# Kernel optimization log

Measured on AMD Instinct MI355X. Metric: run time of the kernel, lower is better.

Reference implementation:

```python
import jax, jax.numpy as jnp
import numpy as np

N_NODES = 50000
N_EDGES = 1600000
N_GRAPHS = 128
EDGE_DIM = 43
IN_DIM = 35
H = 128          # hidden_dim_1 = hidden_dim_2 = hidden_dim_3
G1, G2 = 64, 32  # gate MLP dims
H6, H7, H8 = 256, 128, 64
U0, U1 = 64, 64  # u_shape


def _linear_params(key, out_dim, in_dim):
    k1, k2 = jax.random.split(key)
    bound = 1.0 / np.sqrt(in_dim)
    W = jax.random.uniform(k1, (out_dim, in_dim), minval=-bound, maxval=bound, dtype=jnp.float32)
    b = jax.random.uniform(k2, (out_dim,), minval=-bound, maxval=bound, dtype=jnp.float32)
    return W, b


def setup_inputs() -> dict:
    key = jax.random.key(0)
    ks = jax.random.split(key, 24)
    x = jax.random.normal(ks[0], (N_NODES, IN_DIM), dtype=jnp.float32)
    edge_index = jax.random.randint(ks[1], (2, N_EDGES), 0, N_NODES, dtype=jnp.int64)
    edge_attr = jax.random.normal(ks[2], (N_EDGES, EDGE_DIM), dtype=jnp.float32)
    batch = jnp.sort(jax.random.randint(ks[3], (N_NODES,), 0, N_GRAPHS, dtype=jnp.int64))
    batch = batch.at[0].set(0).at[-1].set(N_GRAPHS - 1)
    u_soap = jax.random.normal(ks[4], (N_GRAPHS, U0), dtype=jnp.float32)
    u_dimer = jax.random.normal(ks[5], (N_GRAPHS, U1), dtype=jnp.float32)

    W1n, b1n = _linear_params(ks[6], H, IN_DIM + EDGE_DIM)
    W1r, b1r = _linear_params(ks[7], H, IN_DIM)
    W2n, b2n = _linear_params(ks[8], H, H + EDGE_DIM)
    W2r, b2r = _linear_params(ks[9], H, H)
    W3n, b3n = _linear_params(ks[10], H, H + EDGE_DIM)
    W3r, b3r = _linear_params(ks[11], H, H)
    Wg1, bg1 = _linear_params(ks[12], G1, H)
    Wg2, bg2 = _linear_params(ks[13], G2, G1)
    Wg3, bg3 = _linear_params(ks[14], 1, G2)
    Wl1, bl1 = _linear_params(ks[15], H6, U0 + U1 + H)
    Wl2, bl2 = _linear_params(ks[16], H7, H6)
    Wl3, bl3 = _linear_params(ks[17], H8, H7)
    Wl, bl = _linear_params(ks[18], 4, H8)

    return dict(x=x, edge_attr=edge_attr, u_soap=u_soap, u_dimer=u_dimer,
                W1n=W1n, b1n=b1n, W1r=W1r, b1r=b1r,
                W2n=W2n, b2n=b2n, W2r=W2r, b2r=b2r,
                W3n=W3n, b3n=b3n, W3r=W3r, b3r=b3r,
                Wg1=Wg1, bg1=bg1, Wg2=Wg2, bg2=bg2, Wg3=Wg3, bg3=bg3,
                Wl1=Wl1, bl1=bl1, Wl2=Wl2, bl2=bl2, Wl3=Wl3, bl3=bl3,
                Wl=Wl, bl=bl,
                edge_index=edge_index, batch=batch)


def _conv(x, src, edge_attr, Wn, bn, Wr, br):
    # gather source nodes, concat edge features, linear + tanh, scatter-add back to SOURCE (as in original)
    x_adj = jnp.tanh(jnp.concatenate([x[src], edge_attr], axis=1) @ Wn.T + bn)  # [E, H]
    neg_sum = jax.ops.segment_sum(x_adj, src, num_segments=N_NODES)             # [N, H]
    return jnp.tanh(x @ Wr.T + br) + neg_sum


def _segment_softmax(gate, batch, num_segments):
    m = jax.ops.segment_max(gate[:, 0], batch, num_segments=num_segments)
    g = jnp.exp(gate[:, 0] - m[batch])
    s = jax.ops.segment_sum(g, batch, num_segments=num_segments)
    return (g / (s[batch] + 1e-16))[:, None]


def reference(x, edge_attr, u_soap, u_dimer,
              W1n, b1n, W1r, b1r, W2n, b2n, W2r, b2r, W3n, b3n, W3r, b3r,
              Wg1, bg1, Wg2, bg2, Wg3, bg3,
              Wl1, bl1, Wl2, bl2, Wl3, bl3, Wl, bl,
              edge_index, batch):
    src = edge_index[0]
    h = _conv(x, src, edge_attr, W1n, b1n, W1r, b1r)
    h = _conv(h, src, edge_attr, W2n, b2n, W2r, b2r)
    h = _conv(h, src, edge_attr, W3n, b3n, W3r, b3r)

    # GlobalAttention readout
    g = jax.nn.relu(h @ Wg1.T + bg1)
    g = jax.nn.relu(g @ Wg2.T + bg2)
    gate = g @ Wg3.T + bg3                             # [N, 1]
    att = _segment_softmax(gate, batch, N_GRAPHS)      # [N, 1]
    embedding = jax.ops.segment_sum(att * h, batch, num_segments=N_GRAPHS)  # [G, H]

    u = jnp.concatenate([u_soap[:, :U0], u_dimer[:, :U1]], axis=1)
    e2 = jnp.concatenate([embedding, u], axis=1)
    out = jax.nn.relu(e2 @ Wl1.T + bl1)
    out = jax.nn.relu(out @ Wl2.T + bl2)
    out = jax.nn.relu(out @ Wl3.T + bl3)
    out4 = out @ Wl.T + bl                             # [G, 4]
    pred_last = out4.sum(axis=1, keepdims=True)
    return jnp.concatenate([out4, pred_last], axis=1), att
```

## Files before the change

kernel.cpp:

```cpp
#include <hip/hip_runtime.h>
#include <cstdint>
#include <cstddef>

#define N_NODES_C 50000
#define N_EDGES_C 1600000
#define N_GRAPHS_C 128
#define EDGE_DIM_C 43
#define IN_DIM_C 35
#define HDIM_C 128
#define MAXG_C 150000

typedef _Float16 f16x8 __attribute__((ext_vector_type(8)));
typedef float f32x4 __attribute__((ext_vector_type(4)));

__device__ __forceinline__ float fast_tanh(float x) {
    float xc = fminf(9.0f, fmaxf(-9.0f, x));
    float t = __expf(2.0f * xc);
    return (t - 1.0f) * __builtin_amdgcn_rcpf(t + 1.0f);
}


__global__ __launch_bounds__(256) void hist_kernel(const int* __restrict__ src,
                                                   int* __restrict__ cnt) {
    int i = blockIdx.x * 256 + threadIdx.x;
    if (i < N_EDGES_C) atomicAdd(&cnt[src[i]], 1);
}

__global__ __launch_bounds__(1024) void scan_kernel(const int* __restrict__ cnt,
                                                    int* __restrict__ rowptr,
                                                    int* __restrict__ work,
                                                    int* __restrict__ growptr,
                                                    int* __restrict__ ngroups) {
    __shared__ int wsumA[16], wsumB[16];
    __shared__ int carryA, carryB;
    int t = threadIdx.x;
    int lane = t & 63, wid = t >> 6;
    if (t == 0) { carryA = 0; carryB = 0; }
    __syncthreads();
    for (int base = 0; base < N_NODES_C; base += 4096) {
        int i0 = base + t * 4;
        int v[4], u[4];
        #pragma unroll
        for (int j = 0; j < 4; ++j) {
            int i = i0 + j;
            v[j] = (i < N_NODES_C) ? cnt[i] : 0;
            u[j] = (v[j] + 15) >> 4;
        }
        int pv[4], pu[4];
        pv[0] = 0; pu[0] = 0;
        #pragma unroll
        for (int j = 1; j < 4; ++j) { pv[j] = pv[j-1] + v[j-1]; pu[j] = pu[j-1] + u[j-1]; }
        int tA = pv[3] + v[3], tB = pu[3] + u[3];
        int x = tA, y = tB;
        #pragma unroll
        for (int off = 1; off < 64; off <<= 1) {
            int xx = __shfl_up(x, off, 64);
            int yy = __shfl_up(y, off, 64);
            if (lane >= off) { x += xx; y += yy; }
        }
        if (lane == 63) { wsumA[wid] = x; wsumB[wid] = y; }
        __syncthreads();
        if (wid == 0) {
            int wa = (lane < 16) ? wsumA[lane] : 0;
            int wb = (lane < 16) ? wsumB[lane] : 0;
            #pragma unroll
            for (int off = 1; off < 16; off <<= 1) {
                int aa = __shfl_up(wa, off, 64);
                int bb = __shfl_up(wb, off, 64);
                if (lane >= off) { wa += aa; wb += bb; }
            }
            if (lane < 16) { wsumA[lane] = wa; wsumB[lane] = wb; }
        }
        __syncthreads();
        int exA = carryA + (wid ? wsumA[wid - 1] : 0) + x - tA;
        int exB = carryB + (wid ? wsumB[wid - 1] : 0) + y - tB;
        #pragma unroll
        for (int j = 0; j < 4; ++j) {
            int i = i0 + j;
            if (i < N_NODES_C) {
                int rv = exA + pv[j];
                rowptr[i] = rv; work[i] = rv;
                growptr[i] = exB + pu[j];
            }
        }
        int totA = wsumA[15], totB = wsumB[15];
        __syncthreads();
        if (t == 0) { carryA += totA; carryB += totB; }
        __syncthreads();
    }
    if (t == 0) {
        rowptr[N_NODES_C] = carryA;
        growptr[N_NODES_C] = carryB;
        ngroups[0] = carryB;
    }
}

__global__ __launch_bounds__(256) void scatter_kernel(const int* __restrict__ src,
                                                      int* __restrict__ work,
                                                      int* __restrict__ perm) {
    int i = blockIdx.x * 256 + threadIdx.x;
    if (i < N_EDGES_C) {
        int s = src[i];
        int pos = atomicAdd(&work[s], 1);
        perm[pos] = i;
    }
}

__global__ __launch_bounds__(256) void graph_misc(const int* __restrict__ rowptr,
                                                  const int* __restrict__ growptr,
                                                  const int* __restrict__ batch,
                                                  int2* __restrict__ nmeta,
                                                  int2* __restrict__ gmeta,
                                                  int* __restrict__ grp) {
    int i = blockIdx.x * 256 + threadIdx.x;
    if (i < N_NODES_C) {
        int r0 = rowptr[i], r1 = rowptr[i + 1];
        int g0 = growptr[i], g1 = growptr[i + 1];
        int deg = r1 - r0;
        nmeta[i] = make_int2(deg, g0);
        for (int g = g0; g < g1; ++g) {
            int o = (g - g0) * 16;
            int vv = deg - o; if (vv > 16) vv = 16;
            gmeta[g] = make_int2(r0 + o, vv);
        }
    }
    if (i <= N_GRAPHS_C) {
        int lo = 0, hi = N_NODES_C;
        while (lo < hi) {
            int mid = (lo + hi) >> 1;
            if (batch[mid] < i) lo = mid + 1; else hi = mid;
        }
        grp[i] = lo;
    }
}

__global__ __launch_bounds__(256) void permute_ea(const float* __restrict__ EA,
                                                  const int* __restrict__ perm,
                                                  const int2* __restrict__ gmeta,
                                                  const int* __restrict__ ngroups_p,
                                                  _Float16* __restrict__ EAp) {
    int t = threadIdx.x;
    int lane = t & 63, wid = t >> 6;
    int row = lane >> 2, q = lane & 3;
    int ng = ngroups_p[0];
    int gstride = gridDim.x * 4;
    for (int g = blockIdx.x * 4 + wid; g < ng; g += gstride) {
        int2 gm = gmeta[g];
        int ebase = gm.x, valid = gm.y;
        bool rv = row < valid;
        int e = rv ? perm[ebase + row] : 0;
        const float* pe = EA + (size_t)e * EDGE_DIM_C;
        unsigned int pk[6];
        #pragma unroll
        for (int jj = 0; jj < 6; ++jj) {
            int c0 = q * 12 + 2 * jj;
            float v0 = (rv && c0 < EDGE_DIM_C) ? pe[c0] : 0.0f;
            float v1 = (rv && c0 + 1 < EDGE_DIM_C) ? pe[c0 + 1] : 0.0f;
            unsigned short h0 = __builtin_bit_cast(unsigned short, (_Float16)v0);
            unsigned short h1 = __builtin_bit_cast(unsigned short, (_Float16)v1);
            pk[jj] = (unsigned int)h0 | ((unsigned int)h1 << 16);
        }
        unsigned int* outp = (unsigned int*)(EAp + (size_t)g * 768 + row * 48 + q * 12);
        *(uint2*)(outp)     = make_uint2(pk[0], pk[1]);
        *(uint2*)(outp + 2) = make_uint2(pk[2], pk[3]);
        *(uint2*)(outp + 4) = make_uint2(pk[4], pk[5]);
    }
}


#define BKN 32
__global__ __launch_bounds__(256) void node_gemm(
    const float* __restrict__ A, int K,
    const float* __restrict__ Wn, int ldn, const float* __restrict__ bn,
    const float* __restrict__ Wr, const float* __restrict__ br,
    float* __restrict__ Base, float* __restrict__ Root)
{
    __shared__ float At[BKN][64];
    __shared__ float Bw[BKN][128];
    int t = threadIdx.x;
    int z = blockIdx.y;
    const float* W = z ? Wr : Wn;
    int ldW = z ? K : ldn;
    const float* bias = z ? br : bn;
    float* Out = z ? Root : Base;

    int m0 = blockIdx.x * 64;
    int tn4 = (t % 32) * 4;
    int tm8 = (t / 32) * 8;
    float acc[8][4];
    #pragma unroll
    for (int a = 0; a < 8; a++)
        #pragma unroll
        for (int b = 0; b < 4; b++) acc[a][b] = 0.0f;

    int nkc = (K + BKN - 1) / BKN;
    for (int c = 0; c < nkc; c++) {
        int kc = c * BKN;
        {
            int m_l = t % 64;
            int kg = t / 64;
            int m = m0 + m_l;
            #pragma unroll
            for (int ii = 0; ii < 8; ii++) {
                int kk = kg * 8 + ii;
                int k = kc + kk;
                float v = 0.0f;
                if (m < N_NODES_C && k < K) v = A[(size_t)m * K + k];
                At[kk][m_l] = v;
            }
        }
        {
            int j = t % 128;
            int kg2 = t / 128;
            #pragma unroll
            for (int ii = 0; ii < 16; ii++) {
                int kk = kg2 * 16 + ii;
                int k = kc + kk;
                float v = 0.0f;
                if (k < K) v = W[(size_t)j * ldW + k];
                Bw[kk][j] = v;
            }
        }
        __syncthreads();
        #pragma unroll
        for (int kk = 0; kk < BKN; kk++) {
            float a[8], b[4];
            #pragma unroll
            for (int mi = 0; mi < 8; mi++) a[mi] = At[kk][tm8 + mi];
            #pragma unroll
            for (int ni = 0; ni < 4; ni++) b[ni] = Bw[kk][tn4 + ni];
            #pragma unroll
            for (int mi = 0; mi < 8; mi++)
                #pragma unroll
                for (int ni = 0; ni < 4; ni++)
                    acc[mi][ni] = fmaf(a[mi], b[ni], acc[mi][ni]);
        }
        __syncthreads();
    }

    float4 bv = *(const float4*)&bias[tn4];
    #pragma unroll
    for (int mi = 0; mi < 8; mi++) {
        int m = m0 + tm8 + mi;
        if (m < N_NODES_C) {
            float4 o;
            o.x = acc[mi][0] + bv.x;
            o.y = acc[mi][1] + bv.y;
            o.z = acc[mi][2] + bv.z;
            o.w = acc[mi][3] + bv.w;
            if (z) { o.x = fast_tanh(o.x); o.y = fast_tanh(o.y); o.z = fast_tanh(o.z); o.w = fast_tanh(o.w); }
            *(float4*)&Out[(size_t)m * HDIM_C + tn4] = o;
        }
    }
}


__global__ __launch_bounds__(256) void edge_mfma(
    const _Float16* __restrict__ EAp, const int2* __restrict__ nmeta,
    const float* __restrict__ Base, const float* __restrict__ Root,
    const float* __restrict__ Wfull, int colOff, int ldW,
    float* __restrict__ Hout)
{
    int t = threadIdx.x;
    int lane = t & 63, wid = t >> 6;
    int l15 = lane & 15, quad = lane >> 4;

    f16x8 bf[8][2];
    #pragma unroll
    for (int nt = 0; nt < 8; ++nt) {
        const float* wr = Wfull + (size_t)(nt * 16 + l15) * ldW + colOff;
        #pragma unroll
        for (int kt = 0; kt < 2; ++kt) {
            f16x8 b;
            #pragma unroll
            for (int j = 0; j < 8; ++j) {
                int k = kt * 32 + quad * 8 + j;
                float v = (k < EDGE_DIM_C) ? wr[k] : 0.0f;
                b[j] = (_Float16)v;
            }
            bf[nt][kt] = b;
        }
    }

    int nstride = gridDim.x * 4;
    for (int n = blockIdx.x * 4 + wid; n < N_NODES_C; n += nstride) {
        int2 nm = nmeta[n];
        int deg = nm.x, gptr = nm.y;
        const float* bp = Base + (size_t)n * HDIM_C;
        float bv[8];
        #pragma unroll
        for (int nt = 0; nt < 8; ++nt) bv[nt] = bp[nt * 16 + l15];
        float cs[8];
        #pragma unroll
        for (int nt = 0; nt < 8; ++nt) cs[nt] = 0.0f;

        int ngr = (deg + 15) >> 4;
        int rbase = quad * 4;
        for (int gi = 0; gi < ngr; ++gi) {
            int valid = deg - gi * 16; if (valid > 16) valid = 16;
            const _Float16* ap = EAp + (size_t)(gptr + gi) * 768 + l15 * 48;
            f16x8 a0 = *(const f16x8*)(ap + quad * 8);
            f16x8 a1;
            if (quad < 2) a1 = *(const f16x8*)(ap + 32 + quad * 8);
            else { f16x8 zz = {}; a1 = zz; }

            f32x4 acc[8];
            #pragma unroll
            for (int nt = 0; nt < 8; ++nt) {
                f32x4 zz = {0.f, 0.f, 0.f, 0.f};
                acc[nt] = __builtin_amdgcn_mfma_f32_16x16x32_f16(a0, bf[nt][0], zz, 0, 0, 0);
                acc[nt] = __builtin_amdgcn_mfma_f32_16x16x32_f16(a1, bf[nt][1], acc[nt], 0, 0, 0);
            }
            #pragma unroll
            for (int nt = 0; nt < 8; ++nt) {
                #pragma unroll
                for (int r = 0; r < 4; ++r) {
                    float v = fast_tanh(acc[nt][r] + bv[nt]);
                    cs[nt] += (rbase + r < valid) ? v : 0.0f;
                }
            }
        }
        #pragma unroll
        for (int nt = 0; nt < 8; ++nt) {
            cs[nt] += __shfl_xor(cs[nt], 16, 64);
            cs[nt] += __shfl_xor(cs[nt], 32, 64);
        }
        float v0, v1;
        if (quad == 0)      { v0 = cs[0]; v1 = cs[1]; }
        else if (quad == 1) { v0 = cs[2]; v1 = cs[3]; }
        else if (quad == 2) { v0 = cs[4]; v1 = cs[5]; }
        else                { v0 = cs[6]; v1 = cs[7]; }
        int c0 = quad * 32 + l15;
        size_t rowb = (size_t)n * HDIM_C;
        Hout[rowb + c0]      = Root[rowb + c0] + v0;
        Hout[rowb + c0 + 16] = Root[rowb + c0 + 16] + v1;
    }
}


__global__ __launch_bounds__(256) void gate_kernel(
    const float* __restrict__ h,
    const float* __restrict__ Wg1, const float* __restrict__ bg1,
    const float* __restrict__ Wg2, const float* __restrict__ bg2,
    const float* __restrict__ Wg3, const float* __restrict__ bg3,
    float* __restrict__ gate)
{
    __shared__ float Ht[128][65];
    __shared__ float G1[64][65];
    __shared__ float G2[32][65];
    int t = threadIdx.x;
    int m0 = blockIdx.x * 64;
    #pragma unroll
    for (int ii = 0; ii < 32; ++ii) {
        int flat = ii * 256 + t;
        int k = flat & 127, m = flat >> 7;
        float v = (m0 + m < N_NODES_C) ? h[(size_t)(m0 + m) * HDIM_C + k] : 0.0f;
        Ht[k][m] = v;
    }
    __syncthreads();
    int m = t & 63, slab = t >> 6;
    {
        float a[16];
        #pragma unroll
        for (int jj = 0; jj < 16; ++jj) a[jj] = bg1[slab * 16 + jj];
        for (int k = 0; k < 128; ++k) {
            float hv = Ht[k][m];
            #pragma unroll
            for (int jj = 0; jj < 16; ++jj)
                a[jj] = fmaf(Wg1[(size_t)(slab * 16 + jj) * 128 + k], hv, a[jj]);
        }
        #pragma unroll
        for (int jj = 0; jj < 16; ++jj) G1[slab * 16 + jj][m] = fmaxf(a[jj], 0.0f);
    }
    __syncthreads();
    {
        float b[8];
        #pragma unroll
        for (int jj = 0; jj < 8; ++jj) b[jj] = bg2[slab * 8 + jj];
        for (int k = 0; k < 64; ++k) {
            float gv = G1[k][m];
            #pragma unroll
            for (int jj = 0; jj < 8; ++jj)
                b[jj] = fmaf(Wg2[(size_t)(slab * 8 + jj) * 64 + k], gv, b[jj]);
        }
        #pragma unroll
        for (int jj = 0; jj < 8; ++jj) G2[slab * 8 + jj][m] = fmaxf(b[jj], 0.0f);
    }
    __syncthreads();
    if (t < 64 && m0 + t < N_NODES_C) {
        float s = bg3[0];
        #pragma unroll
        for (int k = 0; k < 32; ++k) s = fmaf(Wg3[k], G2[k][t], s);
        gate[m0 + t] = s;
    }
}


__global__ __launch_bounds__(256) void graph_attn(
    const float* __restrict__ gate, const int* __restrict__ grp,
    const float* __restrict__ h3, float* __restrict__ att_out,
    float* __restrict__ emb)
{
    int g = blockIdx.x;
    int t = threadIdx.x;
    int s = grp[g], e = grp[g + 1];
    __shared__ float red[256];
    __shared__ float attb[256];

    float m = -3.4e38f;
    for (int i = s + t; i < e; i += 256) m = fmaxf(m, gate[i]);
    red[t] = m;
    __syncthreads();
    #pragma unroll
    for (int off = 128; off >= 1; off >>= 1) {
        if (t < off) red[t] = fmaxf(red[t], red[t + off]);
        __syncthreads();
    }
    m = red[0];
    __syncthreads();

    float sum = 0.0f;
    for (int i = s + t; i < e; i += 256) sum += __expf(gate[i] - m);
    red[t] = sum;
    __syncthreads();
    #pragma unroll
    for (int off = 128; off >= 1; off >>= 1) {
        if (t < off) red[t] += red[t + off];
        __syncthreads();
    }
    float scale = 1.0f / (red[0] + 1e-16f);
    __syncthreads();

    int j = t & 127;
    int half = t >> 7;
    float acc = 0.0f;
    for (int base = s; base < e; base += 256) {
        int i = base + t;
        float a = 0.0f;
        if (i < e) {
            a = __expf(gate[i] - m) * scale;
            att_out[i] = a;
        }
        attb[t] = a;
        __syncthreads();
        int cnt = e - base; if (cnt > 256) cnt = 256;
        for (int r = half; r < cnt; r += 2)
            acc = fmaf(attb[r], h3[(size_t)(base + r) * HDIM_C + j], acc);
        __syncthreads();
    }
    red[t] = acc;
    __syncthreads();
    if (t < 128) emb[(size_t)g * 128 + t] = red[t] + red[t + 128];
}


__global__ __launch_bounds__(256) void final_mlp(
    const float* __restrict__ emb, const float* __restrict__ us, const float* __restrict__ ud,
    const float* __restrict__ Wl1, const float* __restrict__ bl1,
    const float* __restrict__ Wl2, const float* __restrict__ bl2,
    const float* __restrict__ Wl3, const float* __restrict__ bl3,
    const float* __restrict__ Wl, const float* __restrict__ bl,
    float* __restrict__ out5)
{
    int g = blockIdx.x;
    int t = threadIdx.x;
    __shared__ float e2[256], o1[256], o2[128], o3[64], o4[4];
    if (t < 128) e2[t] = emb[(size_t)g * 128 + t];
    else if (t < 192) e2[t] = us[(size_t)g * 64 + (t - 128)];
    else e2[t] = ud[(size_t)g * 64 + (t - 192)];
    __syncthreads();
    {
        float s = bl1[t];
        const float* wr = Wl1 + (size_t)t * 256;
        #pragma unroll 8
        for (int k = 0; k < 256; k++) s = fmaf(wr[k], e2[k], s);
        o1[t] = fmaxf(s, 0.0f);
    }
    __syncthreads();
    if (t < 128) {
        float s = bl2[t];
        const float* wr = Wl2 + (size_t)t * 256;
        #pragma unroll 8
        for (int k = 0; k < 256; k++) s = fmaf(wr[k], o1[k], s);
        o2[t] = fmaxf(s, 0.0f);
    }
    __syncthreads();
    if (t < 64) {
        float s = bl3[t];
        const float* wr = Wl3 + (size_t)t * 128;
        #pragma unroll 8
        for (int k = 0; k < 128; k++) s = fmaf(wr[k], o2[k], s);
        o3[t] = fmaxf(s, 0.0f);
    }
    __syncthreads();
    if (t < 4) {
        float s = bl[t];
        const float* wr = Wl + (size_t)t * 64;
        #pragma unroll 8
        for (int k = 0; k < 64; k++) s = fmaf(wr[k], o3[k], s);
        o4[t] = s;
    }
    __syncthreads();
    if (t < 5) {
        float v = (t < 4) ? o4[t] : (o4[0] + o4[1] + o4[2] + o4[3]);
        out5[(size_t)g * 5 + t] = v;
    }
}


extern "C" void kernel_launch(void* const* d_in, const int* in_sizes, int n_in,
                              void* d_out, int out_size, void* d_ws, size_t ws_size,
                              hipStream_t stream) {
    const float* x       = (const float*)d_in[0];
    const float* ea      = (const float*)d_in[1];
    const float* u_soap  = (const float*)d_in[2];
    const float* u_dimer = (const float*)d_in[3];
    const float* W1n = (const float*)d_in[4];   const float* b1n = (const float*)d_in[5];
    const float* W1r = (const float*)d_in[6];   const float* b1r = (const float*)d_in[7];
    const float* W2n = (const float*)d_in[8];   const float* b2n = (const float*)d_in[9];
    const float* W2r = (const float*)d_in[10];  const float* b2r = (const float*)d_in[11];
    const float* W3n = (const float*)d_in[12];  const float* b3n = (const float*)d_in[13];
    const float* W3r = (const float*)d_in[14];  const float* b3r = (const float*)d_in[15];
    const float* Wg1 = (const float*)d_in[16];  const float* bg1 = (const float*)d_in[17];
    const float* Wg2 = (const float*)d_in[18];  const float* bg2 = (const float*)d_in[19];
    const float* Wg3 = (const float*)d_in[20];  const float* bg3 = (const float*)d_in[21];
    const float* Wl1 = (const float*)d_in[22];  const float* bl1 = (const float*)d_in[23];
    const float* Wl2 = (const float*)d_in[24];  const float* bl2 = (const float*)d_in[25];
    const float* Wl3 = (const float*)d_in[26];  const float* bl3 = (const float*)d_in[27];
    const float* Wl  = (const float*)d_in[28];  const float* bl  = (const float*)d_in[29];
    const int* eidx  = (const int*)d_in[30];
    const int* batch = (const int*)d_in[31];
    const int* src = eidx;

    float* out5 = (float*)d_out;
    float* att  = out5 + (size_t)N_GRAPHS_C * 5;

    char* p = (char*)d_ws;
    size_t off = 0;
    auto alloc = [&](size_t bytes) -> void* {
        void* r = p + off;
        off += (bytes + 255) & ~(size_t)255;
        return r;
    };
    int* cnt     = (int*)alloc((size_t)N_NODES_C * 4);
    int* rowptr  = (int*)alloc((size_t)(N_NODES_C + 1) * 4);
    int* growptr = (int*)alloc((size_t)(N_NODES_C + 1) * 4);
    int* work    = (int*)alloc((size_t)N_NODES_C * 4);
    int* perm    = (int*)alloc((size_t)N_EDGES_C * 4);
    int* grp     = (int*)alloc((size_t)(N_GRAPHS_C + 1) * 4);
    int* ngroups = (int*)alloc(256);
    int2* nmeta  = (int2*)alloc((size_t)N_NODES_C * 8);
    int2* gmeta  = (int2*)alloc((size_t)MAXG_C * 8);
    float* gate  = (float*)alloc((size_t)N_NODES_C * 4);
    float* emb   = (float*)alloc((size_t)N_GRAPHS_C * 128 * 4);
    float* bufP  = (float*)alloc((size_t)N_NODES_C * HDIM_C * 4);
    float* bufQ  = (float*)alloc((size_t)N_NODES_C * HDIM_C * 4);
    float* bufR  = (float*)alloc((size_t)N_NODES_C * HDIM_C * 4);
    _Float16* EAp = (_Float16*)alloc((size_t)MAXG_C * 768 * 2);

    hipMemsetAsync(cnt, 0, (size_t)N_NODES_C * 4, stream);

    int eblocks = (N_EDGES_C + 255) / 256;
    hist_kernel<<<eblocks, 256, 0, stream>>>(src, cnt);
    scan_kernel<<<1, 1024, 0, stream>>>(cnt, rowptr, work, growptr, ngroups);
    scatter_kernel<<<eblocks, 256, 0, stream>>>(src, work, perm);
    graph_misc<<<(N_NODES_C + 255) / 256, 256, 0, stream>>>(rowptr, growptr, batch, nmeta, gmeta, grp);
    permute_ea<<<1536, 256, 0, stream>>>(ea, perm, gmeta, ngroups, EAp);

    dim3 ng((N_NODES_C + 63) / 64, 2);
    int egrid = 2048;

    node_gemm<<<ng, 256, 0, stream>>>(x, IN_DIM_C, W1n, IN_DIM_C + EDGE_DIM_C, b1n, W1r, b1r, bufP, bufQ);
    edge_mfma<<<egrid, 256, 0, stream>>>(EAp, nmeta, bufP, bufQ, W1n, IN_DIM_C, IN_DIM_C + EDGE_DIM_C, bufP);
    node_gemm<<<ng, 256, 0, stream>>>(bufP, HDIM_C, W2n, HDIM_C + EDGE_DIM_C, b2n, W2r, b2r, bufQ, bufR);
    edge_mfma<<<egrid, 256, 0, stream>>>(EAp, nmeta, bufQ, bufR, W2n, HDIM_C, HDIM_C + EDGE_DIM_C, bufQ);
    node_gemm<<<ng, 256, 0, stream>>>(bufQ, HDIM_C, W3n, HDIM_C + EDGE_DIM_C, b3n, W3r, b3r, bufP, bufR);
    edge_mfma<<<egrid, 256, 0, stream>>>(EAp, nmeta, bufP, bufR, W3n, HDIM_C, HDIM_C + EDGE_DIM_C, bufP);

    gate_kernel<<<(N_NODES_C + 63) / 64, 256, 0, stream>>>(bufP, Wg1, bg1, Wg2, bg2, Wg3, bg3, gate);
    graph_attn<<<N_GRAPHS_C, 256, 0, stream>>>(gate, grp, bufP, att, emb);
    final_mlp<<<N_GRAPHS_C, 256, 0, stream>>>(emb, u_soap, u_dimer,
                                              Wl1, bl1, Wl2, bl2, Wl3, bl3, Wl, bl, out5);
}
```

Baseline: 1.860 ms.

## Permute edge attributes by source-order scatter and prefetch next edge group

The edge-attribute packing now scatters: each edge reads its own row contiguously and writes it to its slot in the CSR layout. Before, each destination group gathered edges through a permutation array. This replaces the gmeta construction with an epos array plus a separate pad_zero kernel that clears the unused rows of each node's last group. The node_gemm A-tile load is remapped so each thread reads 8 consecutive k values of one row. The edge_mfma loop now software-prefetches the next group's A fragments so loads overlap the MFMA and tanh work. The cost is an extra kernel launch and scattered writes.

```diff
diff --git a/kernel.cpp b/kernel.cpp
--- a/kernel.cpp
+++ b/kernel.cpp
@@ -97,12 +97,12 @@
 
 __global__ __launch_bounds__(256) void scatter_kernel(const int* __restrict__ src,
                                                       int* __restrict__ work,
-                                                      int* __restrict__ perm) {
+                                                      int* __restrict__ epos) {
     int i = blockIdx.x * 256 + threadIdx.x;
     if (i < N_EDGES_C) {
         int s = src[i];
         int pos = atomicAdd(&work[s], 1);
-        perm[pos] = i;
+        epos[i] = pos;
     }
 }
 
@@ -110,19 +110,11 @@
                                                   const int* __restrict__ growptr,
                                                   const int* __restrict__ batch,
                                                   int2* __restrict__ nmeta,
-                                                  int2* __restrict__ gmeta,
                                                   int* __restrict__ grp) {
     int i = blockIdx.x * 256 + threadIdx.x;
     if (i < N_NODES_C) {
-        int r0 = rowptr[i], r1 = rowptr[i + 1];
-        int g0 = growptr[i], g1 = growptr[i + 1];
-        int deg = r1 - r0;
-        nmeta[i] = make_int2(deg, g0);
-        for (int g = g0; g < g1; ++g) {
-            int o = (g - g0) * 16;
-            int vv = deg - o; if (vv > 16) vv = 16;
-            gmeta[g] = make_int2(r0 + o, vv);
-        }
+        int deg = rowptr[i + 1] - rowptr[i];
+        nmeta[i] = make_int2(deg, growptr[i]);
     }
     if (i <= N_GRAPHS_C) {
         int lo = 0, hi = N_NODES_C;
@@ -134,37 +126,54 @@
     }
 }
 
+__global__ __launch_bounds__(256) void pad_zero(const int2* __restrict__ nmeta,
+                                                _Float16* __restrict__ EAp) {
+    int id = blockIdx.x * 256 + threadIdx.x;
+    int n = id >> 4, row = id & 15;
+    if (n >= N_NODES_C) return;
+    int2 nm = nmeta[n];
+    int deg = nm.x;
+    if (deg == 0) return;
+    int rem = deg & 15;
+    if (rem == 0 || row < rem) return;
+    int g = nm.y + ((deg + 15) >> 4) - 1;
+    uint2* dst = (uint2*)(EAp + (size_t)g * 768 + row * 48);
+    uint2 z = make_uint2(0u, 0u);
+    #pragma unroll
+    for (int j = 0; j < 12; ++j) dst[j] = z;
+}
+
 __global__ __launch_bounds__(256) void permute_ea(const float* __restrict__ EA,
-                                                  const int* __restrict__ perm,
-                                                  const int2* __restrict__ gmeta,
-                                                  const int* __restrict__ ngroups_p,
+                                                  const int* __restrict__ src,
+                                                  const int* __restrict__ epos,
+                                                  const int* __restrict__ rowptr,
+                                                  const int* __restrict__ growptr,
                                                   _Float16* __restrict__ EAp) {
     int t = threadIdx.x;
-    int lane = t & 63, wid = t >> 6;
-    int row = lane >> 2, q = lane & 3;
-    int ng = ngroups_p[0];
-    int gstride = gridDim.x * 4;
-    for (int g = blockIdx.x * 4 + wid; g < ng; g += gstride) {
-        int2 gm = gmeta[g];
-        int ebase = gm.x, valid = gm.y;
-        bool rv = row < valid;
-        int e = rv ? perm[ebase + row] : 0;
-        const float* pe = EA + (size_t)e * EDGE_DIM_C;
-        unsigned int pk[6];
-        #pragma unroll
-        for (int jj = 0; jj < 6; ++jj) {
-            int c0 = q * 12 + 2 * jj;
-            float v0 = (rv && c0 < EDGE_DIM_C) ? pe[c0] : 0.0f;
-            float v1 = (rv && c0 + 1 < EDGE_DIM_C) ? pe[c0 + 1] : 0.0f;
-            unsigned short h0 = __builtin_bit_cast(unsigned short, (_Float16)v0);
-            unsigned short h1 = __builtin_bit_cast(unsigned short, (_Float16)v1);
-            pk[jj] = (unsigned int)h0 | ((unsigned int)h1 << 16);
-        }
-        unsigned int* outp = (unsigned int*)(EAp + (size_t)g * 768 + row * 48 + q * 12);
-        *(uint2*)(outp)     = make_uint2(pk[0], pk[1]);
-        *(uint2*)(outp + 2) = make_uint2(pk[2], pk[3]);
-        *(uint2*)(outp + 4) = make_uint2(pk[4], pk[5]);
-    }
+    int e = blockIdx.x * 64 + (t >> 2);
+    int q = t & 3;
+    if (e >= N_EDGES_C) return;
+    int node = src[e];
+    int pos = epos[e];
+    int r = pos - rowptr[node];
+    int g = growptr[node] + (r >> 4);
+    int row = r & 15;
+
+    const float* pe = EA + (size_t)e * EDGE_DIM_C;
+    unsigned int pk[6];
+    #pragma unroll
+    for (int jj = 0; jj < 6; ++jj) {
+        int c0 = q * 12 + 2 * jj;
+        float v0 = (c0 < EDGE_DIM_C) ? pe[c0] : 0.0f;
+        float v1 = (c0 + 1 < EDGE_DIM_C) ? pe[c0 + 1] : 0.0f;
+        unsigned short h0 = __builtin_bit_cast(unsigned short, (_Float16)v0);
+        unsigned short h1 = __builtin_bit_cast(unsigned short, (_Float16)v1);
+        pk[jj] = (unsigned int)h0 | ((unsigned int)h1 << 16);
+    }
+    unsigned int* outp = (unsigned int*)(EAp + (size_t)g * 768 + row * 48 + q * 12);
+    *(uint2*)(outp)     = make_uint2(pk[0], pk[1]);
+    *(uint2*)(outp + 2) = make_uint2(pk[2], pk[3]);
+    *(uint2*)(outp + 4) = make_uint2(pk[4], pk[5]);
 }
 
 
@@ -197,12 +206,12 @@
     for (int c = 0; c < nkc; c++) {
         int kc = c * BKN;
         {
-            int m_l = t % 64;
-            int kg = t / 64;
+            int m_l = t >> 2;
+            int q = t & 3;
             int m = m0 + m_l;
             #pragma unroll
             for (int ii = 0; ii < 8; ii++) {
-                int kk = kg * 8 + ii;
+                int kk = q * 8 + ii;
                 int k = kc + kk;
                 float v = 0.0f;
                 if (m < N_NODES_C && k < K) v = A[(size_t)m * K + k];
@@ -282,6 +291,10 @@
         }
     }
 
+    int aoff0 = l15 * 48 + quad * 8;
+    int aoff1 = l15 * 48 + 32 + ((quad & 1) * 8);
+    bool useA1 = (quad < 2);
+
     int nstride = gridDim.x * 4;
     for (int n = blockIdx.x * 4 + wid; n < N_NODES_C; n += nstride) {
         int2 nm = nmeta[n];
@@ -296,28 +309,35 @@
 
         int ngr = (deg + 15) >> 4;
         int rbase = quad * 4;
-        for (int gi = 0; gi < ngr; ++gi) {
-            int valid = deg - gi * 16; if (valid > 16) valid = 16;
-            const _Float16* ap = EAp + (size_t)(gptr + gi) * 768 + l15 * 48;
-            f16x8 a0 = *(const f16x8*)(ap + quad * 8);
-            f16x8 a1;
-            if (quad < 2) a1 = *(const f16x8*)(ap + 32 + quad * 8);
-            else { f16x8 zz = {}; a1 = zz; }
-
-            f32x4 acc[8];
-            #pragma unroll
-            for (int nt = 0; nt < 8; ++nt) {
-                f32x4 zz = {0.f, 0.f, 0.f, 0.f};
-                acc[nt] = __builtin_amdgcn_mfma_f32_16x16x32_f16(a0, bf[nt][0], zz, 0, 0, 0);
-                acc[nt] = __builtin_amdgcn_mfma_f32_16x16x32_f16(a1, bf[nt][1], acc[nt], 0, 0, 0);
-            }
-            #pragma unroll
-            for (int nt = 0; nt < 8; ++nt) {
+        if (ngr > 0) {
+            const _Float16* apb = EAp + (size_t)gptr * 768;
+            f16x8 zz8 = {};
+            f16x8 a0 = *(const f16x8*)(apb + aoff0);
+            f16x8 a1 = useA1 ? *(const f16x8*)(apb + aoff1) : zz8;
+            for (int gi = 0; gi < ngr; ++gi) {
+                f16x8 n0 = a0, n1 = a1;
+                if (gi + 1 < ngr) {
+                    const _Float16* apn = apb + (size_t)(gi + 1) * 768;
+                    n0 = *(const f16x8*)(apn + aoff0);
+                    n1 = useA1 ? *(const f16x8*)(apn + aoff1) : zz8;
+                }
+                int valid = deg - gi * 16; if (valid > 16) valid = 16;
+                f32x4 acc[8];
                 #pragma unroll
-                for (int r = 0; r < 4; ++r) {
-                    float v = fast_tanh(acc[nt][r] + bv[nt]);
-                    cs[nt] += (rbase + r < valid) ? v : 0.0f;
+                for (int nt = 0; nt < 8; ++nt) {
+                    f32x4 zz = {0.f, 0.f, 0.f, 0.f};
+                    acc[nt] = __builtin_amdgcn_mfma_f32_16x16x32_f16(a0, bf[nt][0], zz, 0, 0, 0);
+                    acc[nt] = __builtin_amdgcn_mfma_f32_16x16x32_f16(a1, bf[nt][1], acc[nt], 0, 0, 0);
                 }
+                #pragma unroll
+                for (int nt = 0; nt < 8; ++nt) {
+                    #pragma unroll
+                    for (int r = 0; r < 4; ++r) {
+                        float v = fast_tanh(acc[nt][r] + bv[nt]);
+                        cs[nt] += (rbase + r < valid) ? v : 0.0f;
+                    }
+                }
+                a0 = n0; a1 = n1;
             }
         }
         #pragma unroll
@@ -546,11 +566,10 @@
     int* rowptr  = (int*)alloc((size_t)(N_NODES_C + 1) * 4);
     int* growptr = (int*)alloc((size_t)(N_NODES_C + 1) * 4);
     int* work    = (int*)alloc((size_t)N_NODES_C * 4);
-    int* perm    = (int*)alloc((size_t)N_EDGES_C * 4);
+    int* epos    = (int*)alloc((size_t)N_EDGES_C * 4);
     int* grp     = (int*)alloc((size_t)(N_GRAPHS_C + 1) * 4);
     int* ngroups = (int*)alloc(256);
     int2* nmeta  = (int2*)alloc((size_t)N_NODES_C * 8);
-    int2* gmeta  = (int2*)alloc((size_t)MAXG_C * 8);
     float* gate  = (float*)alloc((size_t)N_NODES_C * 4);
     float* emb   = (float*)alloc((size_t)N_GRAPHS_C * 128 * 4);
     float* bufP  = (float*)alloc((size_t)N_NODES_C * HDIM_C * 4);
@@ -563,9 +582,10 @@
     int eblocks = (N_EDGES_C + 255) / 256;
     hist_kernel<<<eblocks, 256, 0, stream>>>(src, cnt);
     scan_kernel<<<1, 1024, 0, stream>>>(cnt, rowptr, work, growptr, ngroups);
-    scatter_kernel<<<eblocks, 256, 0, stream>>>(src, work, perm);
-    graph_misc<<<(N_NODES_C + 255) / 256, 256, 0, stream>>>(rowptr, growptr, batch, nmeta, gmeta, grp);
-    permute_ea<<<1536, 256, 0, stream>>>(ea, perm, gmeta, ngroups, EAp);
+    scatter_kernel<<<eblocks, 256, 0, stream>>>(src, work, epos);
+    graph_misc<<<(N_NODES_C + 255) / 256, 256, 0, stream>>>(rowptr, growptr, batch, nmeta, grp);
+    pad_zero<<<(N_NODES_C * 16 + 255) / 256, 256, 0, stream>>>(nmeta, EAp);
+    permute_ea<<<(N_EDGES_C + 63) / 64, 256, 0, stream>>>(ea, src, epos, rowptr, growptr, EAp);
 
     dim3 ng((N_NODES_C + 63) / 64, 2);
     int egrid = 2048;
```

New measurement: 1.712 ms. 1.09x faster.
